# Kernel tuning notes

Hardware: AMD Instinct MI355X
Metric: run time of the kernel (lower is better)

The kernel has to match this reference:

```python
import jax, jax.numpy as jnp
import numpy as np
import math

TEXT_EMBEDDING_DIM = 768.0
SEQ = 81
DIM = 64
B, H = 256, 16


def setup_inputs() -> dict:
    key = jax.random.key(0)
    kq, kk, kv, ke = jax.random.split(key, 4)
    Q = jax.random.normal(kq, (B, H, SEQ, DIM), dtype=jnp.float32)
    K = jax.random.normal(kk, (B, H, SEQ, DIM), dtype=jnp.float32)
    V = jax.random.normal(kv, (B, H, SEQ, DIM), dtype=jnp.float32)
    emb_table = jax.random.normal(ke, (2 * SEQ + 1, DIM), dtype=jnp.float32)
    return {"Q": Q, "K": K, "V": V, "emb_table": emb_table, "use_causal": 1}


def reference(Q, K, V, emb_table, use_causal):
    S = Q.shape[-2]
    # relative index matrix: rel[i, j] = (S - 1 + i) - j, in [0, 2S-2]
    rel = jnp.arange(S - 1, 2 * S - 1)[:, None] - jnp.arange(S)  # [S, S] int
    emb = emb_table[rel]  # [S, S, d]
    # QK^T plus learned relative-position bias
    eij = jnp.einsum('bhid,bhjd->bhij', Q, K) + jnp.einsum('bhid,ijd->bhij', Q, emb)
    attn = eij / math.sqrt(TEXT_EMBEDDING_DIM)  # note: sqrt(768), not sqrt(dim), per source
    if use_causal:
        i = jnp.arange(S)[:, None]
        j = jnp.arange(S)
        mask = jnp.where(i >= j, 0.0, -1000000000.0).astype(attn.dtype)  # [S, S]
        attn = attn + mask
    attn = jax.nn.softmax(attn, axis=-1)
    return jnp.einsum('bhij,bhjd->bhid', attn, V)
```

## Files before the change

kernel.cpp:

```cpp
#include <hip/hip_runtime.h>
#include <hip/hip_bf16.h>

#define SEQ 81
#define DIM 64
#define NT  384
#define NW  6
#define LDK 68
#define LDV 100
#define LDP 100

typedef short bf16x8 __attribute__((ext_vector_type(8)));
typedef short bf16x4 __attribute__((ext_vector_type(4)));
typedef float f32x4  __attribute__((ext_vector_type(4)));

static constexpr float kS2 = 0.0520587716f;

__device__ __forceinline__ short f2bf(float f) {
    __hip_bfloat16 h = __float2bfloat16(f);
    return __builtin_bit_cast(short, h);
}
__device__ __forceinline__ float bf2f(short h) {
    unsigned u = ((unsigned)(unsigned short)h) << 16;
    return __builtin_bit_cast(float, u);
}
__device__ __forceinline__ bf16x8 cat8(bf16x4 a, bf16x4 b) {
    bf16x8 r;
    r[0]=a[0]; r[1]=a[1]; r[2]=a[2]; r[3]=a[3];
    r[4]=b[0]; r[5]=b[1]; r[6]=b[2]; r[7]=b[3];
    return r;
}

__global__ void emb_cvt_kernel(const float* __restrict__ in, short* __restrict__ out, int n) {
    int i = blockIdx.x * 256 + threadIdx.x;
    if (i < n) out[i] = f2bf(in[i]);
}

__global__ __launch_bounds__(NT, 8)
void rpsa_kernel(const float* __restrict__ Q, const float* __restrict__ K,
                 const float* __restrict__ V, const short* __restrict__ embw,
                 const int* __restrict__ ucp, float* __restrict__ out)
{
    extern __shared__ char smraw[];
    short* sVt = (short*)smraw;
    short* sK  = (short*)(smraw + 12800);
    short* sP  = (short*)(smraw + 12800);

    const int tid = threadIdx.x;
    const size_t base = (size_t)blockIdx.x * (SEQ * DIM);
    const int uc = ucp[0];
    const int w  = tid >> 6, L = tid & 63;
    const int lr = L & 15,  lg = L >> 4;
    const int i0 = 16*w + 4*lg;

    bf16x8 aq0, aq1;
    {
        const int qrow = (16*w + lr < SEQ) ? (16*w + lr) : (SEQ - 1);
        const float* qp = Q + base + qrow*DIM + 8*lg;
        const f32x4 q0 = *(const f32x4*)(qp);
        const f32x4 q1 = *(const f32x4*)(qp + 4);
        const f32x4 q2 = *(const f32x4*)(qp + 32);
        const f32x4 q3 = *(const f32x4*)(qp + 36);
        #pragma unroll
        for (int t = 0; t < 4; ++t) {
            aq0[t]   = f2bf(q0[t]*kS2);
            aq0[4+t] = f2bf(q1[t]*kS2);
            aq1[t]   = f2bf(q2[t]*kS2);
            aq1[4+t] = f2bf(q3[t]*kS2);
        }
    }

    for (int u = tid; u < 96 * DIM / 8; u += NT) {
        const int row = u >> 3, so = (u & 7) * 8;
        bf16x4 lo = {0,0,0,0}, hi = {0,0,0,0};
        if (row < SEQ) {
            const f32x4 k0 = *(const f32x4*)(K + base + row*DIM + so);
            const f32x4 k1 = *(const f32x4*)(K + base + row*DIM + so + 4);
            #pragma unroll
            for (int t = 0; t < 4; ++t) { lo[t] = f2bf(k0[t]); hi[t] = f2bf(k1[t]); }
        }
        *(bf16x4*)(sK + row*LDK + so)     = lo;
        *(bf16x4*)(sK + row*LDK + so + 4) = hi;
    }
    {
        const int j4 = tid >> 4;
        const int d4 = tid & 15;
        f32x4 rw[4];
        #pragma unroll
        for (int e = 0; e < 4; ++e) {
            const int j = 4*j4 + e;
            rw[e] = (j < SEQ) ? *(const f32x4*)(V + base + j*DIM + 4*d4)
                              : (f32x4){0.f,0.f,0.f,0.f};
        }
        #pragma unroll
        for (int c = 0; c < 4; ++c) {
            const int d = 4*d4 + c;
            bf16x4 pv = { f2bf(rw[0][c]), f2bf(rw[1][c]), f2bf(rw[2][c]), f2bf(rw[3][c]) };
            *(bf16x4*)(sVt + d*LDV + 4*j4) = pv;
        }
    }

    bf16x4 qe[NW];
    #pragma unroll
    for (int nt = 0; nt < NW; ++nt) {
        if (nt > w) continue;
        int erow = (SEQ - 1) + 16*nt + lr;
        if (erow > 2*SEQ) erow = 2*SEQ;
        bf16x8 b0 = *(const bf16x8*)(embw + erow*DIM + 8*lg);
        bf16x8 b1 = *(const bf16x8*)(embw + erow*DIM + 32 + 8*lg);
        f32x4 a = {0.f,0.f,0.f,0.f};
        a = __builtin_amdgcn_mfma_f32_16x16x32_bf16(aq0, b0, a, 0, 0, 0);
        a = __builtin_amdgcn_mfma_f32_16x16x32_bf16(aq1, b1, a, 0, 0, 0);
        bf16x4 p = { f2bf(a[0]), f2bf(a[1]), f2bf(a[2]), f2bf(a[3]) };
        qe[nt] = p;
    }
    __syncthreads();

    f32x4 accs[NW] = {};
    const int ntEnd = uc ? w : (NW - 1);
    #pragma unroll
    for (int nt = 0; nt < NW; ++nt) {
        if (nt > ntEnd) continue;
        const int kr = 16*nt + lr;
        bf16x8 b0 = cat8(*(const bf16x4*)(sK + kr*LDK + 8*lg),
                         *(const bf16x4*)(sK + kr*LDK + 8*lg + 4));
        bf16x8 b1 = cat8(*(const bf16x4*)(sK + kr*LDK + 32 + 8*lg),
                         *(const bf16x4*)(sK + kr*LDK + 32 + 8*lg + 4));
        f32x4 a = accs[nt];
        a = __builtin_amdgcn_mfma_f32_16x16x32_bf16(aq0, b0, a, 0, 0, 0);
        a = __builtin_amdgcn_mfma_f32_16x16x32_bf16(aq1, b1, a, 0, 0, 0);
        accs[nt] = a;
    }
    __syncthreads();

    #pragma unroll
    for (int nt = 0; nt < NW; ++nt) {
        if (nt > w) continue;
        #pragma unroll
        for (int r = 0; r < 4; ++r) {
            const int i = i0 + r;
            const int j = i - (16*nt + lr);
            if (j >= 0) sP[i*LDP + j] = qe[nt][r];
        }
    }
    if (!uc) {
        #pragma unroll
        for (int nt = 0; nt < NW; ++nt) {
            if (nt < w) continue;
            const int erow = 16*nt + lr;
            bf16x8 b0 = *(const bf16x8*)(embw + erow*DIM + 8*lg);
            bf16x8 b1 = *(const bf16x8*)(embw + erow*DIM + 32 + 8*lg);
            f32x4 a = {0.f,0.f,0.f,0.f};
            a = __builtin_amdgcn_mfma_f32_16x16x32_bf16(aq0, b0, a, 0, 0, 0);
            a = __builtin_amdgcn_mfma_f32_16x16x32_bf16(aq1, b1, a, 0, 0, 0);
            #pragma unroll
            for (int r = 0; r < 4; ++r) {
                const int i  = i0 + r;
                const int rp = 16*nt + lr;
                if (rp >= i && rp < SEQ - 1)
                    sP[i*LDP + (SEQ - 1 + i - rp)] = f2bf(a[r]);
            }
        }
    }

    float mr[4] = {-1e30f, -1e30f, -1e30f, -1e30f};
    #pragma unroll
    for (int nt = 0; nt < NW; ++nt) {
        if (uc && nt > w) continue;
        const int j = 16*nt + lr;
        #pragma unroll
        for (int r = 0; r < 4; ++r) {
            const int i = i0 + r;
            float v = accs[nt][r] + bf2f(sP[i*LDP + j]);
            accs[nt][r] = v;
            const int jl = uc ? ((i < SEQ-1) ? i : SEQ-1) : (SEQ-1);
            if (j <= jl) mr[r] = fmaxf(mr[r], v);
        }
    }
    #pragma unroll
    for (int r = 0; r < 4; ++r) {
        float m = mr[r];
        m = fmaxf(m, __shfl_xor(m, 1, 16));
        m = fmaxf(m, __shfl_xor(m, 2, 16));
        m = fmaxf(m, __shfl_xor(m, 4, 16));
        m = fmaxf(m, __shfl_xor(m, 8, 16));
        mr[r] = m;
    }
    float sr[4] = {0.f, 0.f, 0.f, 0.f};
    #pragma unroll
    for (int nt = 0; nt < NW; ++nt) {
        if (uc && nt > w) continue;
        const int j = 16*nt + lr;
        #pragma unroll
        for (int r = 0; r < 4; ++r) {
            const int i = i0 + r;
            const int jl = uc ? ((i < SEQ-1) ? i : SEQ-1) : (SEQ-1);
            const float e = (j <= jl) ? exp2f(accs[nt][r] - mr[r]) : 0.f;
            accs[nt][r] = e; sr[r] += e;
        }
    }
    #pragma unroll
    for (int r = 0; r < 4; ++r) {
        float s = sr[r];
        s += __shfl_xor(s, 1, 16);
        s += __shfl_xor(s, 2, 16);
        s += __shfl_xor(s, 4, 16);
        s += __shfl_xor(s, 8, 16);
        sr[r] = 1.f / s;
    }
    #pragma unroll
    for (int nt = 0; nt < NW; ++nt) {
        const int j = 16*nt + lr;
        #pragma unroll
        for (int r = 0; r < 4; ++r) {
            const int i = i0 + r;
            sP[i*LDP + j] = f2bf(accs[nt][r] * sr[r]);
        }
    }

    bf16x8 ap0, ap1, ap2;
    {
        const int row = 16*w + lr;
        ap0 = cat8(*(const bf16x4*)(sP + row*LDP + 8*lg),
                   *(const bf16x4*)(sP + row*LDP + 8*lg + 4));
        ap1 = cat8(*(const bf16x4*)(sP + row*LDP + 32 + 8*lg),
                   *(const bf16x4*)(sP + row*LDP + 32 + 8*lg + 4));
        ap2 = cat8(*(const bf16x4*)(sP + row*LDP + 64 + 8*lg),
                   *(const bf16x4*)(sP + row*LDP + 64 + 8*lg + 4));
    }
    #pragma unroll
    for (int nt = 0; nt < 4; ++nt) {
        const int d = 16*nt + lr;
        bf16x8 b0 = cat8(*(const bf16x4*)(sVt + d*LDV + 8*lg),
                         *(const bf16x4*)(sVt + d*LDV + 8*lg + 4));
        bf16x8 b1 = cat8(*(const bf16x4*)(sVt + d*LDV + 32 + 8*lg),
                         *(const bf16x4*)(sVt + d*LDV + 32 + 8*lg + 4));
        bf16x8 b2 = cat8(*(const bf16x4*)(sVt + d*LDV + 64 + 8*lg),
                         *(const bf16x4*)(sVt + d*LDV + 64 + 8*lg + 4));
        f32x4 a = {0.f,0.f,0.f,0.f};
        a = __builtin_amdgcn_mfma_f32_16x16x32_bf16(ap0, b0, a, 0, 0, 0);
        a = __builtin_amdgcn_mfma_f32_16x16x32_bf16(ap1, b1, a, 0, 0, 0);
        a = __builtin_amdgcn_mfma_f32_16x16x32_bf16(ap2, b2, a, 0, 0, 0);
        #pragma unroll
        for (int r = 0; r < 4; ++r) {
            const int i = i0 + r;
            if (i < SEQ) out[base + i*DIM + 16*nt + lr] = a[r];
        }
    }
}

extern "C" void kernel_launch(void* const* d_in, const int* in_sizes, int n_in,
                              void* d_out, int out_size, void* d_ws, size_t ws_size,
                              hipStream_t stream) {
    const float* Q   = (const float*)d_in[0];
    const float* K   = (const float*)d_in[1];
    const float* V   = (const float*)d_in[2];
    const float* emb = (const float*)d_in[3];
    const int*   uc  = (const int*)d_in[4];
    float* out = (float*)d_out;

    const int nbh   = in_sizes[0] / (SEQ * DIM);
    const int n_emb = in_sizes[3];

    short* embw = (short*)d_ws;
    emb_cvt_kernel<<<(n_emb + 255) / 256, 256, 0, stream>>>(emb, embw, n_emb);

    const size_t smem = 32000;
    hipFuncSetAttribute(reinterpret_cast<const void*>(rpsa_kernel),
                        hipFuncAttributeMaxDynamicSharedMemorySize, (int)smem);
    rpsa_kernel<<<nbh, NT, smem, stream>>>(Q, K, V, embw, uc, out);
}
```

Baseline: 86.73 us.

## Transpose MFMA outputs so each lane owns a query row; drop max-subtraction and defer normalization

Swaps the A/B operands of every MFMA so each lane holds four consecutive key columns of a single query row. Row reductions then need only two cross-lane shuffles, and P can be written to LDS as packed bf16x4. Softmax no longer subtracts the row max, and the 1/sum normalization moves to the PV output, which is also stored as contiguous float4. This removes one reduction pass and a rescale pass, and widens global stores. Without max-subtraction, exp2 can overflow for large logits; that is safe only because the scaled inputs are small.

```diff
diff --git a/kernel.cpp b/kernel.cpp
--- a/kernel.cpp
+++ b/kernel.cpp
@@ -50,11 +50,11 @@
     const int uc = ucp[0];
     const int w  = tid >> 6, L = tid & 63;
     const int lr = L & 15,  lg = L >> 4;
-    const int i0 = 16*w + 4*lg;
+    const int iRow = 16*w + lr;
 
     bf16x8 aq0, aq1;
     {
-        const int qrow = (16*w + lr < SEQ) ? (16*w + lr) : (SEQ - 1);
+        const int qrow = (iRow < SEQ) ? iRow : (SEQ - 1);
         const float* qp = Q + base + qrow*DIM + 8*lg;
         const f32x4 q0 = *(const f32x4*)(qp);
         const f32x4 q1 = *(const f32x4*)(qp + 4);
@@ -101,17 +101,17 @@
 
     bf16x4 qe[NW];
     #pragma unroll
-    for (int nt = 0; nt < NW; ++nt) {
-        if (nt > w) continue;
-        int erow = (SEQ - 1) + 16*nt + lr;
+    for (int nt2 = 0; nt2 < NW; ++nt2) {
+        if (nt2 > w) continue;
+        int erow = 80 + 16*nt2 + lr;
         if (erow > 2*SEQ) erow = 2*SEQ;
-        bf16x8 b0 = *(const bf16x8*)(embw + erow*DIM + 8*lg);
-        bf16x8 b1 = *(const bf16x8*)(embw + erow*DIM + 32 + 8*lg);
+        bf16x8 e0 = *(const bf16x8*)(embw + erow*DIM + 8*lg);
+        bf16x8 e1 = *(const bf16x8*)(embw + erow*DIM + 32 + 8*lg);
         f32x4 a = {0.f,0.f,0.f,0.f};
-        a = __builtin_amdgcn_mfma_f32_16x16x32_bf16(aq0, b0, a, 0, 0, 0);
-        a = __builtin_amdgcn_mfma_f32_16x16x32_bf16(aq1, b1, a, 0, 0, 0);
+        a = __builtin_amdgcn_mfma_f32_16x16x32_bf16(e0, aq0, a, 0, 0, 0);
+        a = __builtin_amdgcn_mfma_f32_16x16x32_bf16(e1, aq1, a, 0, 0, 0);
         bf16x4 p = { f2bf(a[0]), f2bf(a[1]), f2bf(a[2]), f2bf(a[3]) };
-        qe[nt] = p;
+        qe[nt2] = p;
     }
     __syncthreads();
 
@@ -126,106 +126,72 @@
         bf16x8 b1 = cat8(*(const bf16x4*)(sK + kr*LDK + 32 + 8*lg),
                          *(const bf16x4*)(sK + kr*LDK + 32 + 8*lg + 4));
         f32x4 a = accs[nt];
-        a = __builtin_amdgcn_mfma_f32_16x16x32_bf16(aq0, b0, a, 0, 0, 0);
-        a = __builtin_amdgcn_mfma_f32_16x16x32_bf16(aq1, b1, a, 0, 0, 0);
+        a = __builtin_amdgcn_mfma_f32_16x16x32_bf16(b0, aq0, a, 0, 0, 0);
+        a = __builtin_amdgcn_mfma_f32_16x16x32_bf16(b1, aq1, a, 0, 0, 0);
         accs[nt] = a;
     }
     __syncthreads();
 
     #pragma unroll
-    for (int nt = 0; nt < NW; ++nt) {
-        if (nt > w) continue;
+    for (int nt2 = 0; nt2 < NW; ++nt2) {
+        if (nt2 > w) continue;
         #pragma unroll
         for (int r = 0; r < 4; ++r) {
-            const int i = i0 + r;
-            const int j = i - (16*nt + lr);
-            if (j >= 0) sP[i*LDP + j] = qe[nt][r];
+            const int j = 16*(w - nt2) + lr - 4*lg - r;
+            if (j >= 0) sP[iRow*LDP + j] = qe[nt2][r];
         }
     }
     if (!uc) {
         #pragma unroll
-        for (int nt = 0; nt < NW; ++nt) {
-            if (nt < w) continue;
-            const int erow = 16*nt + lr;
-            bf16x8 b0 = *(const bf16x8*)(embw + erow*DIM + 8*lg);
-            bf16x8 b1 = *(const bf16x8*)(embw + erow*DIM + 32 + 8*lg);
+        for (int nt2 = 0; nt2 < NW - 1; ++nt2) {
+            if (nt2 < w) continue;
+            const int erow = 16*nt2 + lr;
+            bf16x8 e0 = *(const bf16x8*)(embw + erow*DIM + 8*lg);
+            bf16x8 e1 = *(const bf16x8*)(embw + erow*DIM + 32 + 8*lg);
             f32x4 a = {0.f,0.f,0.f,0.f};
-            a = __builtin_amdgcn_mfma_f32_16x16x32_bf16(aq0, b0, a, 0, 0, 0);
-            a = __builtin_amdgcn_mfma_f32_16x16x32_bf16(aq1, b1, a, 0, 0, 0);
+            a = __builtin_amdgcn_mfma_f32_16x16x32_bf16(e0, aq0, a, 0, 0, 0);
+            a = __builtin_amdgcn_mfma_f32_16x16x32_bf16(e1, aq1, a, 0, 0, 0);
             #pragma unroll
             for (int r = 0; r < 4; ++r) {
-                const int i  = i0 + r;
-                const int rp = 16*nt + lr;
-                if (rp >= i && rp < SEQ - 1)
-                    sP[i*LDP + (SEQ - 1 + i - rp)] = f2bf(a[r]);
+                const int rel = 16*nt2 + 4*lg + r;
+                if (rel >= iRow) sP[iRow*LDP + (80 + iRow - rel)] = f2bf(a[r]);
             }
         }
     }
 
-    float mr[4] = {-1e30f, -1e30f, -1e30f, -1e30f};
+    const int jmax = uc ? ((iRow < SEQ-1) ? iRow : SEQ-1) : (SEQ-1);
+    float sum = 0.f;
     #pragma unroll
     for (int nt = 0; nt < NW; ++nt) {
-        if (uc && nt > w) continue;
-        const int j = 16*nt + lr;
-        #pragma unroll
-        for (int r = 0; r < 4; ++r) {
-            const int i = i0 + r;
-            float v = accs[nt][r] + bf2f(sP[i*LDP + j]);
-            accs[nt][r] = v;
-            const int jl = uc ? ((i < SEQ-1) ? i : SEQ-1) : (SEQ-1);
-            if (j <= jl) mr[r] = fmaxf(mr[r], v);
-        }
-    }
-    #pragma unroll
-    for (int r = 0; r < 4; ++r) {
-        float m = mr[r];
-        m = fmaxf(m, __shfl_xor(m, 1, 16));
-        m = fmaxf(m, __shfl_xor(m, 2, 16));
-        m = fmaxf(m, __shfl_xor(m, 4, 16));
-        m = fmaxf(m, __shfl_xor(m, 8, 16));
-        mr[r] = m;
-    }
-    float sr[4] = {0.f, 0.f, 0.f, 0.f};
-    #pragma unroll
-    for (int nt = 0; nt < NW; ++nt) {
-        if (uc && nt > w) continue;
-        const int j = 16*nt + lr;
-        #pragma unroll
-        for (int r = 0; r < 4; ++r) {
-            const int i = i0 + r;
-            const int jl = uc ? ((i < SEQ-1) ? i : SEQ-1) : (SEQ-1);
-            const float e = (j <= jl) ? exp2f(accs[nt][r] - mr[r]) : 0.f;
-            accs[nt][r] = e; sr[r] += e;
-        }
-    }
-    #pragma unroll
-    for (int r = 0; r < 4; ++r) {
-        float s = sr[r];
-        s += __shfl_xor(s, 1, 16);
-        s += __shfl_xor(s, 2, 16);
-        s += __shfl_xor(s, 4, 16);
-        s += __shfl_xor(s, 8, 16);
-        sr[r] = 1.f / s;
-    }
-    #pragma unroll
-    for (int nt = 0; nt < NW; ++nt) {
-        const int j = 16*nt + lr;
-        #pragma unroll
-        for (int r = 0; r < 4; ++r) {
-            const int i = i0 + r;
-            sP[i*LDP + j] = f2bf(accs[nt][r] * sr[r]);
-        }
-    }
+        short* slot = sP + iRow*LDP + 16*nt + 4*lg;
+        if (nt <= ntEnd) {
+            bf16x4 bias = *(const bf16x4*)(slot);
+            bf16x4 p;
+            #pragma unroll
+            for (int r = 0; r < 4; ++r) {
+                const int j = 16*nt + 4*lg + r;
+                const float x = accs[nt][r] + bf2f(bias[r]);
+                const float e = (j <= jmax) ? exp2f(x) : 0.f;
+                sum += e;
+                p[r] = f2bf(e);
+            }
+            *(bf16x4*)(slot) = p;
+        } else {
+            *(bf16x4*)(slot) = (bf16x4){0,0,0,0};
+        }
+    }
+    sum += __shfl_xor(sum, 16);
+    sum += __shfl_xor(sum, 32);
+    const float inv = 1.f / sum;
 
     bf16x8 ap0, ap1, ap2;
     {
-        const int row = 16*w + lr;
-        ap0 = cat8(*(const bf16x4*)(sP + row*LDP + 8*lg),
-                   *(const bf16x4*)(sP + row*LDP + 8*lg + 4));
-        ap1 = cat8(*(const bf16x4*)(sP + row*LDP + 32 + 8*lg),
-                   *(const bf16x4*)(sP + row*LDP + 32 + 8*lg + 4));
-        ap2 = cat8(*(const bf16x4*)(sP + row*LDP + 64 + 8*lg),
-                   *(const bf16x4*)(sP + row*LDP + 64 + 8*lg + 4));
+        ap0 = cat8(*(const bf16x4*)(sP + iRow*LDP + 8*lg),
+                   *(const bf16x4*)(sP + iRow*LDP + 8*lg + 4));
+        ap1 = cat8(*(const bf16x4*)(sP + iRow*LDP + 32 + 8*lg),
+                   *(const bf16x4*)(sP + iRow*LDP + 32 + 8*lg + 4));
+        ap2 = cat8(*(const bf16x4*)(sP + iRow*LDP + 64 + 8*lg),
+                   *(const bf16x4*)(sP + iRow*LDP + 64 + 8*lg + 4));
     }
     #pragma unroll
     for (int nt = 0; nt < 4; ++nt) {
@@ -237,13 +203,12 @@
         bf16x8 b2 = cat8(*(const bf16x4*)(sVt + d*LDV + 64 + 8*lg),
                          *(const bf16x4*)(sVt + d*LDV + 64 + 8*lg + 4));
         f32x4 a = {0.f,0.f,0.f,0.f};
-        a = __builtin_amdgcn_mfma_f32_16x16x32_bf16(ap0, b0, a, 0, 0, 0);
-        a = __builtin_amdgcn_mfma_f32_16x16x32_bf16(ap1, b1, a, 0, 0, 0);
-        a = __builtin_amdgcn_mfma_f32_16x16x32_bf16(ap2, b2, a, 0, 0, 0);
-        #pragma unroll
-        for (int r = 0; r < 4; ++r) {
-            const int i = i0 + r;
-            if (i < SEQ) out[base + i*DIM + 16*nt + lr] = a[r];
+        a = __builtin_amdgcn_mfma_f32_16x16x32_bf16(b0, ap0, a, 0, 0, 0);
+        a = __builtin_amdgcn_mfma_f32_16x16x32_bf16(b1, ap1, a, 0, 0, 0);
+        a = __builtin_amdgcn_mfma_f32_16x16x32_bf16(b2, ap2, a, 0, 0, 0);
+        if (iRow < SEQ) {
+            f32x4 o = { a[0]*inv, a[1]*inv, a[2]*inv, a[3]*inv };
+            *(f32x4*)(out + base + iRow*DIM + 16*nt + 4*lg) = o;
         }
     }
 }
```

After: 83.85 us. 3.3% less time.
